# Kernel optimization log

Hardware: AMD Instinct MI355X
Metric: run time of the kernel (lower is better)

The kernel has to match this reference:

```python
import math
import jax
import jax.numpy as jnp
import numpy as np

SEGMENT_SIZE = 2048   # w (init: segment_size)
DILATION_RATE = 4     # r (init: dilation_rate)
D_MODEL = 1024        # init: d_model


def _sparse_indices(n: int, w: int, r: int, head_idx: int) -> np.ndarray:
    """Static SparsifyIndices: per segment of size w, take tokens offset::r.
    Since r divides w, every segment yields exactly m=w//r indices (no -1 pad).
    Returns flat global token indices, shape (S*m,)."""
    S = n // w
    m = w // r
    off = head_idx % r
    seg_start = np.arange(S, dtype=np.int64)[:, None] * w      # (S,1)
    within = off + r * np.arange(m, dtype=np.int64)[None, :]   # (1,m)
    return (seg_start + within).reshape(-1)


def setup_inputs() -> dict:
    key = jax.random.key(0)
    x = jax.random.normal(key, (4, 8192, D_MODEL), dtype=jnp.float32)
    return {"x": x, "head_idx": 1}


def reference(x, head_idx):
    b, n0, d = x.shape
    w, r = SEGMENT_SIZE, DILATION_RATE
    pad = (-n0) % w
    if pad:
        x = jnp.pad(x, ((0, 0), (0, pad), (0, 0)))
    n = n0 + pad
    idx = _sparse_indices(n, w, r, int(head_idx))  # static, (S*m,)
    S, m = n // w, w // r

    # Gather dilated tokens per segment: (b, S, m, d)
    xg = x[:, idx, :].reshape(b, S, m, d)

    # Softmax attention within each sub-segment (q=k=v=xg)
    scores = jnp.einsum('bsid,bsjd->bsij', xg, xg) / math.sqrt(d)  # (b,S,m,m)
    probs = jax.nn.softmax(scores, axis=-1)
    att = jnp.einsum('bsij,bsjd->bsid', probs, xg).reshape(b, S * m, d)

    # MixOutputs: alpha-weighted scatter-add back to full sequence
    denoms = att.sum(-1)                                       # (b, S*m)
    denom_sums = jnp.zeros((b, n), x.dtype).at[:, idx].add(denoms)
    alphas = denoms / denom_sums[:, idx]                       # (b, S*m)
    out = jnp.zeros((b, n, d), x.dtype).at[:, idx, :].add(att * alphas[..., None])
    return out
```

## Files before the change

### kernel.cpp

```cpp
#include <hip/hip_runtime.h>
#include <hip/hip_bf16.h>


typedef __bf16 bf16_t;
typedef __bf16 bf16x8 __attribute__((ext_vector_type(8)));
typedef float floatx4 __attribute__((ext_vector_type(4)));

#define D_MODEL 1024
#define SEG_W   2048
#define RATE    4
#define M_SUB   512
#define NTOK    8192
#define NSEGT   16
#define XG_ELEMS ((long)NSEGT * M_SUB * D_MODEL)

__device__ __forceinline__ void gload16(const bf16_t* g, bf16_t* l) {
    __builtin_amdgcn_global_load_lds(
        (const __attribute__((address_space(1))) void*)g,
        (__attribute__((address_space(3))) void*)l, 16, 0, 0);
}

__global__ __launch_bounds__(256) void gather_kernel(
    const float* __restrict__ x, const int* __restrict__ hidp,
    bf16_t* __restrict__ xg, bf16_t* __restrict__ xgT)
{
    const int off = ((hidp[0] % RATE) + RATE) % RATE;
    const int bid = blockIdx.x;
    const int seg = bid >> 7;
    const int rem = bid & 127;
    const int it  = rem >> 4;
    const int dt  = rem & 15;
    const int b   = seg >> 2, s = seg & 3;

    __shared__ ushort tile[64][65];

    const int t  = threadIdx.x;
    const int r  = t >> 2;
    const int cq = (t & 3) << 4;

    union U8 { bf16x8 v; ushort u[8]; };

    {
        const int  i   = it * 64 + r;
        const long tok = (long)s * SEG_W + off + 4L * i;
        const float* src = x + ((long)b * NTOK + tok) * D_MODEL + dt * 64 + cq;
        float4 f0 = ((const float4*)src)[0];
        float4 f1 = ((const float4*)src)[1];
        float4 f2 = ((const float4*)src)[2];
        float4 f3 = ((const float4*)src)[3];
        U8 lo, hi;
        lo.v[0]=(bf16_t)f0.x; lo.v[1]=(bf16_t)f0.y; lo.v[2]=(bf16_t)f0.z; lo.v[3]=(bf16_t)f0.w;
        lo.v[4]=(bf16_t)f1.x; lo.v[5]=(bf16_t)f1.y; lo.v[6]=(bf16_t)f1.z; lo.v[7]=(bf16_t)f1.w;
        hi.v[0]=(bf16_t)f2.x; hi.v[1]=(bf16_t)f2.y; hi.v[2]=(bf16_t)f2.z; hi.v[3]=(bf16_t)f2.w;
        hi.v[4]=(bf16_t)f3.x; hi.v[5]=(bf16_t)f3.y; hi.v[6]=(bf16_t)f3.z; hi.v[7]=(bf16_t)f3.w;
        bf16_t* dstg = xg + ((long)seg * M_SUB + i) * D_MODEL + dt * 64 + cq;
        *(bf16x8*)(dstg)     = lo.v;
        *(bf16x8*)(dstg + 8) = hi.v;
        #pragma unroll
        for (int j = 0; j < 8; ++j) { tile[r][cq + j] = lo.u[j]; tile[r][cq + 8 + j] = hi.u[j]; }
    }
    __syncthreads();
    {
        const int dc = r;
        const int iq = cq;
        U8 o0, o1;
        #pragma unroll
        for (int j = 0; j < 8; ++j) { o0.u[j] = tile[iq + j][dc]; o1.u[j] = tile[iq + 8 + j][dc]; }
        bf16_t* dstT = xgT + ((long)seg * D_MODEL + dt * 64 + dc) * M_SUB + it * 64 + iq;
        *(bf16x8*)(dstT)     = o0.v;
        *(bf16x8*)(dstT + 8) = o1.v;
    }
}

__global__ __launch_bounds__(256) void qk_kernel(
    const bf16_t* __restrict__ xg, bf16_t* __restrict__ S)
{
    const int bid = blockIdx.x;
    const int seg = bid >> 5;
    const int mt  = (bid >> 2) & 7;
    const int nt  = bid & 3;

    const int tid  = threadIdx.x;
    const int w    = tid >> 6;
    const int lane = tid & 63;
    const int l16  = lane & 15;
    const int quad = lane >> 4;
    const int wr   = w >> 1, wc = w & 1;
    const int rowin = lane >> 3;
    const int cswz  = ((lane & 7) ^ rowin) * 8;
    const int rsw   = l16 & 7;

    __shared__ alignas(16) bf16_t As[64 * 64];
    __shared__ alignas(16) bf16_t Bs[128 * 64];

    const bf16_t* xseg = xg + (long)seg * M_SUB * D_MODEL;

    const bf16_t* ga0 = xseg + (long)(mt * 64 + w * 16 + rowin) * D_MODEL + cswz;
    const bf16_t* ga1 = ga0 + 8 * D_MODEL;
    const bf16_t* gb0 = xseg + (long)(nt * 128 + w * 32 + rowin) * D_MODEL + cswz;
    const bf16_t* gb1 = gb0 +  8 * D_MODEL;
    const bf16_t* gb2 = gb0 + 16 * D_MODEL;
    const bf16_t* gb3 = gb0 + 24 * D_MODEL;
    bf16_t* la0 = &As[(w * 16 + 0) * 64];
    bf16_t* la1 = &As[(w * 16 + 8) * 64];
    bf16_t* lb0 = &Bs[(w * 32 + 0) * 64];
    bf16_t* lb1 = &Bs[(w * 32 + 8) * 64];
    bf16_t* lb2 = &Bs[(w * 32 + 16) * 64];
    bf16_t* lb3 = &Bs[(w * 32 + 24) * 64];

    floatx4 acc[2][4];
    #pragma unroll
    for (int i = 0; i < 2; ++i)
        #pragma unroll
        for (int j = 0; j < 4; ++j) acc[i][j] = (floatx4){0.f, 0.f, 0.f, 0.f};

    for (int kk = 0; kk < D_MODEL; kk += 64) {
        __syncthreads();
        gload16(ga0 + kk, la0); gload16(ga1 + kk, la1);
        gload16(gb0 + kk, lb0); gload16(gb1 + kk, lb1);
        gload16(gb2 + kk, lb2); gload16(gb3 + kk, lb3);
        __syncthreads();

        #pragma unroll
        for (int ks = 0; ks < 2; ++ks) {
            bf16x8 Af[2], Bf[4];
            #pragma unroll
            for (int m2 = 0; m2 < 2; ++m2) {
                const int row = wr * 32 + m2 * 16 + l16;
                Af[m2] = *(const bf16x8*)&As[row * 64 + (((ks * 4 + quad) ^ rsw) * 8)];
            }
            #pragma unroll
            for (int n2 = 0; n2 < 4; ++n2) {
                const int row = wc * 64 + n2 * 16 + l16;
                Bf[n2] = *(const bf16x8*)&Bs[row * 64 + (((ks * 4 + quad) ^ rsw) * 8)];
            }
            #pragma unroll
            for (int m2 = 0; m2 < 2; ++m2)
                #pragma unroll
                for (int n2 = 0; n2 < 4; ++n2)
                    acc[m2][n2] = __builtin_amdgcn_mfma_f32_16x16x32_bf16(Af[m2], Bf[n2], acc[m2][n2], 0, 0, 0);
        }
    }

    const float scale = 0.03125f;
    bf16_t* Sseg = S + (long)seg * M_SUB * M_SUB;
    #pragma unroll
    for (int m2 = 0; m2 < 2; ++m2) {
        const int qrow = mt * 64 + wr * 32 + m2 * 16 + quad * 4;
        #pragma unroll
        for (int n2 = 0; n2 < 4; ++n2) {
            const int col = nt * 128 + wc * 64 + n2 * 16 + l16;
            #pragma unroll
            for (int rg = 0; rg < 4; ++rg)
                Sseg[(long)(qrow + rg) * M_SUB + col] = (bf16_t)(acc[m2][n2][rg] * scale);
        }
    }
}

__global__ __launch_bounds__(256) void pv_fused_kernel(
    const bf16_t* __restrict__ S, const bf16_t* __restrict__ xgT,
    const int* __restrict__ hidp, float* __restrict__ out)
{
    const int off = ((hidp[0] % RATE) + RATE) % RATE;
    const int bid = blockIdx.x;
    const int seg = bid >> 6;
    const int mt  = (bid >> 3) & 7;
    const int nt  = bid & 7;
    const int b   = seg >> 2, s = seg & 3;

    const int tid  = threadIdx.x;
    const int w    = tid >> 6;
    const int lane = tid & 63;
    const int l16  = lane & 15;
    const int quad = lane >> 4;
    const int wr   = w >> 1, wc = w & 1;
    const int rowin = lane >> 3;
    const int cswz  = ((lane & 7) ^ rowin) * 8;
    const int rsw   = l16 & 7;

    __shared__ alignas(16) bf16_t Stile[64 * 512];
    __shared__ alignas(16) bf16_t Bs[128 * 64];

    const bf16_t* Srow0 = S + (long)seg * M_SUB * M_SUB + (long)(mt * 64) * M_SUB;
    #pragma unroll
    for (int i = 0; i < 16; ++i) {
        const int row = w * 16 + i;
        const bf16_t* g = Srow0 + (long)row * M_SUB + ((lane ^ (i & 7)) * 8);
        gload16(g, &Stile[row * 512]);
    }
    __syncthreads();

    {
        const int sub = lane >> 5;
        const int c   = lane & 31;
        #pragma unroll
        for (int pass = 0; pass < 8; ++pass) {
            const int row = w * 16 + pass * 2 + sub;
            bf16_t* p0 = &Stile[row * 512 + c * 8];
            bf16_t* p1 = &Stile[row * 512 + (c + 32) * 8];
            bf16x8 v0 = *(const bf16x8*)p0;
            bf16x8 v1 = *(const bf16x8*)p1;
            float f[16];
            #pragma unroll
            for (int j = 0; j < 8; ++j) { f[j] = (float)v0[j]; f[8 + j] = (float)v1[j]; }
            float m = f[0];
            #pragma unroll
            for (int j = 1; j < 16; ++j) m = fmaxf(m, f[j]);
            #pragma unroll
            for (int d = 1; d < 32; d <<= 1) m = fmaxf(m, __shfl_xor(m, d, 64));
            float sum = 0.f;
            #pragma unroll
            for (int j = 0; j < 16; ++j) { f[j] = __expf(f[j] - m); sum += f[j]; }
            #pragma unroll
            for (int d = 1; d < 32; d <<= 1) sum += __shfl_xor(sum, d, 64);
            const float inv = 1.0f / sum;
            #pragma unroll
            for (int j = 0; j < 8; ++j) { v0[j] = (bf16_t)(f[j] * inv); v1[j] = (bf16_t)(f[8 + j] * inv); }
            *(bf16x8*)p0 = v0;
            *(bf16x8*)p1 = v1;
        }
    }
    __syncthreads();

    const bf16_t* Bseg = xgT + (long)seg * D_MODEL * M_SUB + (long)nt * 128 * M_SUB;
    const bf16_t* gb0 = Bseg + (long)(w * 32 + rowin) * M_SUB + cswz;
    const bf16_t* gb1 = gb0 +  8 * M_SUB;
    const bf16_t* gb2 = gb0 + 16 * M_SUB;
    const bf16_t* gb3 = gb0 + 24 * M_SUB;
    bf16_t* lb0 = &Bs[(w * 32 + 0) * 64];
    bf16_t* lb1 = &Bs[(w * 32 + 8) * 64];
    bf16_t* lb2 = &Bs[(w * 32 + 16) * 64];
    bf16_t* lb3 = &Bs[(w * 32 + 24) * 64];

    floatx4 acc[2][4];
    #pragma unroll
    for (int i = 0; i < 2; ++i)
        #pragma unroll
        for (int j = 0; j < 4; ++j) acc[i][j] = (floatx4){0.f, 0.f, 0.f, 0.f};

    for (int kk = 0; kk < M_SUB; kk += 64) {
        __syncthreads();
        gload16(gb0 + kk, lb0); gload16(gb1 + kk, lb1);
        gload16(gb2 + kk, lb2); gload16(gb3 + kk, lb3);
        __syncthreads();

        const int kchunk = kk >> 3;
        #pragma unroll
        for (int ks = 0; ks < 2; ++ks) {
            bf16x8 Af[2], Bf[4];
            #pragma unroll
            for (int m2 = 0; m2 < 2; ++m2) {
                const int row = wr * 32 + m2 * 16 + l16;
                Af[m2] = *(const bf16x8*)&Stile[row * 512 + (kchunk | ((ks * 4 + quad) ^ rsw)) * 8];
            }
            #pragma unroll
            for (int n2 = 0; n2 < 4; ++n2) {
                const int row = wc * 64 + n2 * 16 + l16;
                Bf[n2] = *(const bf16x8*)&Bs[row * 64 + (((ks * 4 + quad) ^ rsw) * 8)];
            }
            #pragma unroll
            for (int m2 = 0; m2 < 2; ++m2)
                #pragma unroll
                for (int n2 = 0; n2 < 4; ++n2)
                    acc[m2][n2] = __builtin_amdgcn_mfma_f32_16x16x32_bf16(Af[m2], Bf[n2], acc[m2][n2], 0, 0, 0);
        }
    }

    float* obase = out + (long)b * NTOK * D_MODEL;
    #pragma unroll
    for (int m2 = 0; m2 < 2; ++m2) {
        const int qrow0 = mt * 64 + wr * 32 + m2 * 16 + quad * 4;
        #pragma unroll
        for (int rg = 0; rg < 4; ++rg) {
            const long tok = (long)s * SEG_W + off + 4L * (qrow0 + rg);
            float* orow = obase + tok * D_MODEL;
            #pragma unroll
            for (int n2 = 0; n2 < 4; ++n2) {
                const int d = nt * 128 + wc * 64 + n2 * 16 + l16;
                __builtin_nontemporal_store(acc[m2][n2][rg], &orow[d]);
            }
        }
    }

    {
        const floatx4 z = {0.f, 0.f, 0.f, 0.f};
        const int zr = tid >> 5;
        const int zc = tid & 31;
        #pragma unroll 4
        for (int p = 0; p < 24; ++p) {
            const int j = p * 8 + zr;
            const int q = j / 3, e = j % 3;
            const int delta = e + (e >= off ? 1 : 0);
            const long tok = (long)s * SEG_W + 4L * (mt * 64 + q) + delta;
            float* dst = obase + tok * D_MODEL + nt * 128 + zc * 4;
            __builtin_nontemporal_store(z, (floatx4*)dst);
        }
    }
}

extern "C" void kernel_launch(void* const* d_in, const int* in_sizes, int n_in,
                              void* d_out, int out_size, void* d_ws, size_t ws_size,
                              hipStream_t stream) {
    const float* x   = (const float*)d_in[0];
    const int*   hid = (const int*)d_in[1];
    float*       out = (float*)d_out;
    bf16_t* xg  = (bf16_t*)d_ws;
    bf16_t* xgT = xg + XG_ELEMS;
    bf16_t* S   = xgT + XG_ELEMS;

    gather_kernel<<<dim3(2048), dim3(256), 0, stream>>>(x, hid, xg, xgT);
    qk_kernel<<<dim3(512), dim3(256), 0, stream>>>(xg, S);
    pv_fused_kernel<<<dim3(1024), dim3(256), 0, stream>>>(S, xgT, hid, out);
}
```

Measured before the change: 250.8 us.

## Split softmax into its own kernel and fold QK scale into gather

Softmax moves out of the PV kernel into a standalone row-wise kernel. Before, each of the 8 column-tile blocks sharing a row tile recomputed the same softmax, so the work was done 8 times over; now each row is normalised once and the PV kernel just loads probabilities. The 1/sqrt(d) scale is split as sqrt(1/32) applied to the bf16 xg copy used for QK, which removes the epilogue multiply. The cost is an extra launch plus an extra global read and write of the score matrix, and slightly different bf16 rounding of the scaled Q/K.

```diff
diff --git a/kernel.cpp b/kernel.cpp
--- a/kernel.cpp
+++ b/kernel.cpp
@@ -13,6 +13,7 @@
 #define NTOK    8192
 #define NSEGT   16
 #define XG_ELEMS ((long)NSEGT * M_SUB * D_MODEL)
+#define QK_SCALE 0.17677669529663689f
 
 __device__ __forceinline__ void gload16(const bf16_t* g, bf16_t* l) {
     __builtin_amdgcn_global_load_lds(
@@ -48,14 +49,22 @@
         float4 f1 = ((const float4*)src)[1];
         float4 f2 = ((const float4*)src)[2];
         float4 f3 = ((const float4*)src)[3];
-        U8 lo, hi;
+        U8 lo, hi, ls, hs;
         lo.v[0]=(bf16_t)f0.x; lo.v[1]=(bf16_t)f0.y; lo.v[2]=(bf16_t)f0.z; lo.v[3]=(bf16_t)f0.w;
         lo.v[4]=(bf16_t)f1.x; lo.v[5]=(bf16_t)f1.y; lo.v[6]=(bf16_t)f1.z; lo.v[7]=(bf16_t)f1.w;
         hi.v[0]=(bf16_t)f2.x; hi.v[1]=(bf16_t)f2.y; hi.v[2]=(bf16_t)f2.z; hi.v[3]=(bf16_t)f2.w;
         hi.v[4]=(bf16_t)f3.x; hi.v[5]=(bf16_t)f3.y; hi.v[6]=(bf16_t)f3.z; hi.v[7]=(bf16_t)f3.w;
+        ls.v[0]=(bf16_t)(f0.x*QK_SCALE); ls.v[1]=(bf16_t)(f0.y*QK_SCALE);
+        ls.v[2]=(bf16_t)(f0.z*QK_SCALE); ls.v[3]=(bf16_t)(f0.w*QK_SCALE);
+        ls.v[4]=(bf16_t)(f1.x*QK_SCALE); ls.v[5]=(bf16_t)(f1.y*QK_SCALE);
+        ls.v[6]=(bf16_t)(f1.z*QK_SCALE); ls.v[7]=(bf16_t)(f1.w*QK_SCALE);
+        hs.v[0]=(bf16_t)(f2.x*QK_SCALE); hs.v[1]=(bf16_t)(f2.y*QK_SCALE);
+        hs.v[2]=(bf16_t)(f2.z*QK_SCALE); hs.v[3]=(bf16_t)(f2.w*QK_SCALE);
+        hs.v[4]=(bf16_t)(f3.x*QK_SCALE); hs.v[5]=(bf16_t)(f3.y*QK_SCALE);
+        hs.v[6]=(bf16_t)(f3.z*QK_SCALE); hs.v[7]=(bf16_t)(f3.w*QK_SCALE);
         bf16_t* dstg = xg + ((long)seg * M_SUB + i) * D_MODEL + dt * 64 + cq;
-        *(bf16x8*)(dstg)     = lo.v;
-        *(bf16x8*)(dstg + 8) = hi.v;
+        *(bf16x8*)(dstg)     = ls.v;
+        *(bf16x8*)(dstg + 8) = hs.v;
         #pragma unroll
         for (int j = 0; j < 8; ++j) { tile[r][cq + j] = lo.u[j]; tile[r][cq + 8 + j] = hi.u[j]; }
     }
@@ -142,7 +151,6 @@
         }
     }
 
-    const float scale = 0.03125f;
     bf16_t* Sseg = S + (long)seg * M_SUB * M_SUB;
     #pragma unroll
     for (int m2 = 0; m2 < 2; ++m2) {
@@ -152,13 +160,38 @@
             const int col = nt * 128 + wc * 64 + n2 * 16 + l16;
             #pragma unroll
             for (int rg = 0; rg < 4; ++rg)
-                Sseg[(long)(qrow + rg) * M_SUB + col] = (bf16_t)(acc[m2][n2][rg] * scale);
-        }
-    }
-}
-
-__global__ __launch_bounds__(256) void pv_fused_kernel(
-    const bf16_t* __restrict__ S, const bf16_t* __restrict__ xgT,
+                Sseg[(long)(qrow + rg) * M_SUB + col] = (bf16_t)acc[m2][n2][rg];
+        }
+    }
+}
+
+__global__ __launch_bounds__(256) void softmax_kernel(bf16_t* __restrict__ S)
+{
+    const int row  = blockIdx.x * 4 + (threadIdx.x >> 6);
+    const int lane = threadIdx.x & 63;
+    bf16_t* p = S + (long)row * M_SUB + lane * 8;
+    bf16x8 v = *(const bf16x8*)p;
+    float f[8];
+    #pragma unroll
+    for (int j = 0; j < 8; ++j) f[j] = (float)v[j];
+    float m = f[0];
+    #pragma unroll
+    for (int j = 1; j < 8; ++j) m = fmaxf(m, f[j]);
+    #pragma unroll
+    for (int d = 1; d < 64; d <<= 1) m = fmaxf(m, __shfl_xor(m, d, 64));
+    float sum = 0.f;
+    #pragma unroll
+    for (int j = 0; j < 8; ++j) { f[j] = __expf(f[j] - m); sum += f[j]; }
+    #pragma unroll
+    for (int d = 1; d < 64; d <<= 1) sum += __shfl_xor(sum, d, 64);
+    const float inv = 1.0f / sum;
+    #pragma unroll
+    for (int j = 0; j < 8; ++j) v[j] = (bf16_t)(f[j] * inv);
+    *(bf16x8*)p = v;
+}
+
+__global__ __launch_bounds__(256) void pv_kernel(
+    const bf16_t* __restrict__ P, const bf16_t* __restrict__ xgT,
     const int* __restrict__ hidp, float* __restrict__ out)
 {
     const int off = ((hidp[0] % RATE) + RATE) % RATE;
@@ -181,46 +214,13 @@
     __shared__ alignas(16) bf16_t Stile[64 * 512];
     __shared__ alignas(16) bf16_t Bs[128 * 64];
 
-    const bf16_t* Srow0 = S + (long)seg * M_SUB * M_SUB + (long)(mt * 64) * M_SUB;
+    const bf16_t* Prow0 = P + (long)seg * M_SUB * M_SUB + (long)(mt * 64) * M_SUB;
     #pragma unroll
     for (int i = 0; i < 16; ++i) {
         const int row = w * 16 + i;
-        const bf16_t* g = Srow0 + (long)row * M_SUB + ((lane ^ (i & 7)) * 8);
+        const bf16_t* g = Prow0 + (long)row * M_SUB + ((lane ^ (i & 7)) * 8);
         gload16(g, &Stile[row * 512]);
     }
-    __syncthreads();
-
-    {
-        const int sub = lane >> 5;
-        const int c   = lane & 31;
-        #pragma unroll
-        for (int pass = 0; pass < 8; ++pass) {
-            const int row = w * 16 + pass * 2 + sub;
-            bf16_t* p0 = &Stile[row * 512 + c * 8];
-            bf16_t* p1 = &Stile[row * 512 + (c + 32) * 8];
-            bf16x8 v0 = *(const bf16x8*)p0;
-            bf16x8 v1 = *(const bf16x8*)p1;
-            float f[16];
-            #pragma unroll
-            for (int j = 0; j < 8; ++j) { f[j] = (float)v0[j]; f[8 + j] = (float)v1[j]; }
-            float m = f[0];
-            #pragma unroll
-            for (int j = 1; j < 16; ++j) m = fmaxf(m, f[j]);
-            #pragma unroll
-            for (int d = 1; d < 32; d <<= 1) m = fmaxf(m, __shfl_xor(m, d, 64));
-            float sum = 0.f;
-            #pragma unroll
-            for (int j = 0; j < 16; ++j) { f[j] = __expf(f[j] - m); sum += f[j]; }
-            #pragma unroll
-            for (int d = 1; d < 32; d <<= 1) sum += __shfl_xor(sum, d, 64);
-            const float inv = 1.0f / sum;
-            #pragma unroll
-            for (int j = 0; j < 8; ++j) { v0[j] = (bf16_t)(f[j] * inv); v1[j] = (bf16_t)(f[8 + j] * inv); }
-            *(bf16x8*)p0 = v0;
-            *(bf16x8*)p1 = v1;
-        }
-    }
-    __syncthreads();
 
     const bf16_t* Bseg = xgT + (long)seg * D_MODEL * M_SUB + (long)nt * 128 * M_SUB;
     const bf16_t* gb0 = Bseg + (long)(w * 32 + rowin) * M_SUB + cswz;
@@ -310,5 +310,6 @@
 
     gather_kernel<<<dim3(2048), dim3(256), 0, stream>>>(x, hid, xg, xgT);
     qk_kernel<<<dim3(512), dim3(256), 0, stream>>>(xg, S);
-    pv_fused_kernel<<<dim3(1024), dim3(256), 0, stream>>>(S, xgT, hid, out);
-}
+    softmax_kernel<<<dim3(2048), dim3(256), 0, stream>>>(S);
+    pv_kernel<<<dim3(1024), dim3(256), 0, stream>>>(S, xgT, hid, out);
+}
```

After: 251.9 us. Within noise of the previous version (+0.5%).
